# Kernel tuning notes

Hardware: AMD Instinct MI355X
Metric: run time of the kernel (lower is better)

## Reference

```python
import jax, jax.numpy as jnp
import numpy as np

N_NODES = 10000
SEQ_LEN = 50


def setup_inputs() -> dict:
    key = jax.random.key(0)
    ks = jax.random.split(key, 12)
    B, IN, H, E = 2, 128, 64, 160000
    s = 0.05
    return {
        "x": jax.random.normal(ks[0], (B, IN), jnp.float32),
        "src": jax.random.randint(ks[1], (E,), 0, N_NODES, jnp.int32),
        "dst": jax.random.randint(ks[2], (E,), 0, N_NODES, jnp.int32),
        "w_r_w": jax.random.normal(ks[3], (IN, H), jnp.float32) * s,
        "w_r_b": jnp.zeros((H,), jnp.float32),
        "w_z_w": jax.random.normal(ks[4], (IN, H), jnp.float32) * s,
        "w_z_b": jnp.zeros((H,), jnp.float32),
        "w_h_w": jax.random.normal(ks[5], (IN, H), jnp.float32) * s,
        "w_h_b": jnp.zeros((H,), jnp.float32),
        "gcn_w": jax.random.normal(ks[6], (H, H), jnp.float32) * s,
        "gcn_b": jnp.zeros((H,), jnp.float32),
    }


def reference(x, src, dst, w_r_w, w_r_b, w_z_w, w_z_b, w_h_w, w_h_b, gcn_w, gcn_b):
    B = x.shape[0]
    H = gcn_w.shape[0]
    N = N_NODES
    ones = jnp.ones(src.shape, jnp.float32)
    deg_out = jax.ops.segment_sum(ones, src, num_segments=N)
    deg_in = jax.ops.segment_sum(ones, dst, num_segments=N)
    norm_s = jnp.clip(deg_out, 1.0) ** -0.5  # [N]
    norm_d = jnp.clip(deg_in, 1.0) ** -0.5   # [N]

    def gcn(h):  # h: [B, N, H] -> symmetric-normalized GraphConv (DGL norm='both')
        hs = h * norm_s[None, :, None]
        msg = jnp.take(hs, src, axis=1).swapaxes(0, 1)        # [E, B, H]
        agg = jax.ops.segment_sum(msg, dst, num_segments=N)   # [N, B, H]
        agg = (agg * norm_d[:, None, None]).swapaxes(0, 1)    # [B, N, H]
        return agg @ gcn_w + gcn_b

    # time-invariant input projections (x is fixed across timesteps)
    xr = (x @ w_r_w + w_r_b)[:, None, :]  # [B, 1, H]
    xz = (x @ w_z_w + w_z_b)[:, None, :]
    xh = (x @ w_h_w + w_h_b)[:, None, :]

    h0 = jnp.zeros((B, N, H), jnp.float32)

    def step(h, _):
        g = gcn(h)  # identical for all three gate uses
        r = jax.nn.sigmoid(xr + g)
        z = jax.nn.sigmoid(xz + g)
        h_tilde = jnp.tanh(xh + r * g)
        h_new = (1.0 - z) * h + z * h_tilde
        return h_new, h_new

    _, outs = jax.lax.scan(step, h0, None, length=SEQ_LEN)  # [T, B, N, H]
    return outs.transpose(1, 0, 2, 3)                        # [B, T, N, H]
```

## Files before the change

### kernel.cpp

```cpp
#include <hip/hip_runtime.h>
#include <cstdint>
#include <cstddef>

#define NNODES 10000
#define HDIM 64
#define INDIM 128
#define TSTEPS 50

__device__ __forceinline__ float sigmoidf_(float x){ return 1.0f/(1.0f+__expf(-x)); }
__device__ __forceinline__ float tanhf_(float x){ float e=__expf(2.0f*x); return 1.0f-2.0f/(e+1.0f); }

__device__ __forceinline__ uint32_t pack_bf16x2(float a, float b){
  uint32_t ua = __float_as_uint(a), ub = __float_as_uint(b);
  ua = (ua + 0x7fffu + ((ua>>16)&1u)) >> 16;
  ub = (ub + 0x7fffu + ((ub>>16)&1u)) >> 16;
  return ua | (ub<<16);
}

__global__ void hist_kernel(const int* __restrict__ src, const int* __restrict__ dst,
                            int* __restrict__ deg_out, int* __restrict__ deg_in, int E){
  int e = blockIdx.x*blockDim.x + threadIdx.x;
  if (e < E){
    atomicAdd(&deg_out[src[e]], 1);
    atomicAdd(&deg_in[dst[e]], 1);
  }
}

__global__ void scan_kernel(const int* __restrict__ deg_in, const int* __restrict__ deg_out,
                            int* __restrict__ row_off, int* __restrict__ cursor,
                            float* __restrict__ norm_s, float* __restrict__ norm_d){
  __shared__ int part[256];
  int tid = threadIdx.x;
  const int CH = (NNODES + 255)/256;
  int base = tid*CH;
  int local = 0;
  for (int k=0;k<CH;k++){ int n=base+k; if(n<NNODES) local += (deg_in[n]+7)&~7; }
  part[tid]=local;
  __syncthreads();
  if (tid==0){
    int run=0;
    for(int i=0;i<256;i++){ int t=part[i]; part[i]=run; run+=t; }
  }
  __syncthreads();
  int run = part[tid];
  for (int k=0;k<CH;k++){
    int n=base+k;
    if (n<NNODES){
      int di = deg_in[n];
      row_off[n]=run; cursor[n]=run;
      run += (di+7)&~7;
      norm_d[n] = rsqrtf(fmaxf((float)di,1.0f));
      norm_s[n] = rsqrtf(fmaxf((float)deg_out[n],1.0f));
    }
  }
  if (tid==255) row_off[NNODES]=run;
}

__global__ void fill_kernel(const int* __restrict__ src, const int* __restrict__ dst,
                            int* __restrict__ cursor, uint32_t* __restrict__ csrb, int E){
  int e = blockIdx.x*blockDim.x + threadIdx.x;
  if (e<E){
    int pos = atomicAdd(&cursor[dst[e]],1);
    csrb[pos] = (uint32_t)src[e]*256u;
  }
}

__global__ void pad_kernel(const int* __restrict__ row_off, const int* __restrict__ cursor,
                           uint32_t* __restrict__ csrb){
  int n = blockIdx.x*blockDim.x + threadIdx.x;
  if (n < NNODES){
    int q  = cursor[n];
    int qe = row_off[n+1];
    for (; q < qe; ++q) csrb[q] = (uint32_t)NNODES*256u;
  }
}

__global__ void xproj_kernel(const float* __restrict__ x,
                             const float* __restrict__ wr, const float* __restrict__ br,
                             const float* __restrict__ wz, const float* __restrict__ bz,
                             const float* __restrict__ wh, const float* __restrict__ bh,
                             float* __restrict__ xproj){
  int tid = threadIdx.x;
  if (tid >= 384) return;
  int g = tid >> 7; int r = tid & 127; int b = r >> 6; int i = r & 63;
  const float* w  = (g==0)?wr:(g==1)?wz:wh;
  const float* bb = (g==0)?br:(g==1)?bz:bh;
  float s = bb[i];
  for (int k=0;k<INDIM;k++) s = fmaf(x[b*INDIM+k], w[k*HDIM+i], s);
  xproj[g*128 + i*2 + b] = s;
}

__global__ void transpose_w_kernel(const float* __restrict__ gcn_w, float* __restrict__ wT){
  int tid = threadIdx.x;
  for (int k=0;k<16;k++){
    int idx = tid*16 + k;
    int i = idx >> 6, j = idx & 63;
    wT[idx] = gcn_w[j*HDIM + i];
  }
}

#define ACC8(A0,A1,A2,A3,q0,q1,q2,q3,q4,q5,q6,q7) do{ \
  A0.x += __uint_as_float((q0)<<16); A0.y += __uint_as_float((q0)&0xffff0000u); \
  A1.x += __uint_as_float((q1)<<16); A1.y += __uint_as_float((q1)&0xffff0000u); \
  A2.x += __uint_as_float((q2)<<16); A2.y += __uint_as_float((q2)&0xffff0000u); \
  A3.x += __uint_as_float((q3)<<16); A3.y += __uint_as_float((q3)&0xffff0000u); \
  A0.x += __uint_as_float((q4)<<16); A0.y += __uint_as_float((q4)&0xffff0000u); \
  A1.x += __uint_as_float((q5)<<16); A1.y += __uint_as_float((q5)&0xffff0000u); \
  A2.x += __uint_as_float((q6)<<16); A2.y += __uint_as_float((q6)&0xffff0000u); \
  A3.x += __uint_as_float((q7)<<16); A3.y += __uint_as_float((q7)&0xffff0000u); \
}while(0)

#define GATHER8(cp,it,P0,P1,P2,P3,P4,P5,P6,P7) \
  uint4 oa##P0 = (cp)[2*(it)], ob##P0 = (cp)[2*(it)+1]; \
  uint32_t P0 = *(const uint32_t*)(ybb+oa##P0.x); \
  uint32_t P1 = *(const uint32_t*)(ybb+oa##P0.y); \
  uint32_t P2 = *(const uint32_t*)(ybb+oa##P0.z); \
  uint32_t P3 = *(const uint32_t*)(ybb+oa##P0.w); \
  uint32_t P4 = *(const uint32_t*)(ybb+ob##P0.x); \
  uint32_t P5 = *(const uint32_t*)(ybb+ob##P0.y); \
  uint32_t P6 = *(const uint32_t*)(ybb+ob##P0.z); \
  uint32_t P7 = *(const uint32_t*)(ybb+ob##P0.w);

__launch_bounds__(512, 6)
__global__ void step_kernel(const float2* __restrict__ h_in, float2* __restrict__ h_out,
                            const uint32_t* __restrict__ yb_in, uint32_t* __restrict__ yb_out,
                            float* __restrict__ out, int t,
                            const int* __restrict__ row_off, const uint32_t* __restrict__ csrb,
                            const float* __restrict__ norm_d, const float* __restrict__ norm_s,
                            const float* __restrict__ wT, const float* __restrict__ gcn_b,
                            const float2* __restrict__ xproj){
  __shared__ __align__(16) float4 wlds[64][16];
  __shared__ __align__(16) float2 hstage[8][2][64];

  const int tid  = threadIdx.x;
  const int lane = tid & 63;
  const int wv   = tid >> 6;

  {
    const float4* wt4 = (const float4*)wT;
    #pragma unroll
    for (int q=0;q<2;q++){
      int c = tid*2 + q;
      int l = c >> 4, kk = c & 15;
      int swl = (l & 15) ^ (((l>>4)&1) << 2);
      wlds[l][kk ^ swl] = wt4[c];
    }
  }

  const int wid = __builtin_amdgcn_readfirstlane(blockIdx.x*8 + wv);
  const int n0 = wid, n1 = wid + 5000;

  int beg0 = __builtin_amdgcn_readfirstlane(row_off[n0]);
  int end0 = __builtin_amdgcn_readfirstlane(row_off[n0+1]);
  int beg1 = __builtin_amdgcn_readfirstlane(row_off[n1]);
  int end1 = __builtin_amdgcn_readfirstlane(row_off[n1+1]);

  float2 hold0 = h_in[(size_t)n0*HDIM + lane];
  float2 hold1 = h_in[(size_t)n1*HDIM + lane];

  const char* ybb = (const char*)yb_in + (uint32_t)(lane*4);
  const uint4* cp0 = (const uint4*)(csrb + beg0);
  const uint4* cp1 = (const uint4*)(csrb + beg1);
  const int it0 = (end0-beg0)>>3;
  const int it1 = (end1-beg1)>>3;
  const int itc = it0 < it1 ? it0 : it1;

  float2 A0{0.f,0.f},A1{0.f,0.f},A2{0.f,0.f},A3{0.f,0.f};
  float2 B0{0.f,0.f},B1{0.f,0.f},B2{0.f,0.f},B3{0.f,0.f};

  int it = 0;
  #pragma unroll 1
  for (; it<itc; ++it){
    GATHER8(cp0,it,p0,p1,p2,p3,p4,p5,p6,p7);
    GATHER8(cp1,it,q0,q1,q2,q3,q4,q5,q6,q7);
    ACC8(A0,A1,A2,A3,p0,p1,p2,p3,p4,p5,p6,p7);
    ACC8(B0,B1,B2,B3,q0,q1,q2,q3,q4,q5,q6,q7);
  }
  #pragma unroll 1
  for (int ia=it; ia<it0; ++ia){
    GATHER8(cp0,ia,p0,p1,p2,p3,p4,p5,p6,p7);
    ACC8(A0,A1,A2,A3,p0,p1,p2,p3,p4,p5,p6,p7);
  }
  #pragma unroll 1
  for (int ib=it; ib<it1; ++ib){
    GATHER8(cp1,ib,q0,q1,q2,q3,q4,q5,q6,q7);
    ACC8(B0,B1,B2,B3,q0,q1,q2,q3,q4,q5,q6,q7);
  }

  float s00 = (A0.x+A1.x)+(A2.x+A3.x), s01 = (A0.y+A1.y)+(A2.y+A3.y);
  float s10 = (B0.x+B1.x)+(B2.x+B3.x), s11 = (B0.y+B1.y)+(B2.y+B3.y);

  const float  bias = gcn_b[lane];
  const float2 xrv  = xproj[lane];
  const float2 xzv  = xproj[64+lane];
  const float2 xhv  = xproj[128+lane];
  const float  nd0  = norm_d[n0], ns0 = norm_s[n0];
  const float  nd1  = norm_d[n1], ns1 = norm_s[n1];

  float g00 = fmaf(nd0, s00, bias), g01 = fmaf(nd0, s01, bias);
  float g10 = fmaf(nd1, s10, bias), g11 = fmaf(nd1, s11, bias);

  float r00 = sigmoidf_(xrv.x+g00), r01 = sigmoidf_(xrv.y+g01);
  float r10 = sigmoidf_(xrv.x+g10), r11 = sigmoidf_(xrv.y+g11);
  float z00 = sigmoidf_(xzv.x+g00), z01 = sigmoidf_(xzv.y+g01);
  float z10 = sigmoidf_(xzv.x+g10), z11 = sigmoidf_(xzv.y+g11);
  float t00 = tanhf_(xhv.x+r00*g00), t01 = tanhf_(xhv.y+r01*g01);
  float t10 = tanhf_(xhv.x+r10*g10), t11 = tanhf_(xhv.y+r11*g11);
  float h00 = hold0.x + z00*(t00 - hold0.x);
  float h01 = hold0.y + z01*(t01 - hold0.y);
  float h10 = hold1.x + z10*(t10 - hold1.x);
  float h11 = hold1.y + z11*(t11 - hold1.y);

  const size_t NH = (size_t)NNODES*HDIM;
  h_out[(size_t)n0*HDIM + lane] = make_float2(h00,h01);
  h_out[(size_t)n1*HDIM + lane] = make_float2(h10,h11);
  size_t idx0 = (size_t)t*NH + (size_t)n0*HDIM + lane;
  size_t idx1 = (size_t)t*NH + (size_t)n1*HDIM + lane;
  __builtin_nontemporal_store(h00, &out[idx0]);
  __builtin_nontemporal_store(h01, &out[(size_t)TSTEPS*NH + idx0]);
  __builtin_nontemporal_store(h10, &out[idx1]);
  __builtin_nontemporal_store(h11, &out[(size_t)TSTEPS*NH + idx1]);

  hstage[wv][0][lane] = make_float2(h00,h01);
  hstage[wv][1][lane] = make_float2(h10,h11);
  __syncthreads();

  const int sl = (lane & 15) ^ (((lane>>4)&1) << 2);
  const float4* hp0 = (const float4*)hstage[wv][0];
  const float4* hp1 = (const float4*)hstage[wv][1];
  float y00=0.f, y01=0.f, y10=0.f, y11=0.f;
  #pragma unroll
  for (int kk=0;kk<16;kk++){
    float4 w4  = wlds[lane][kk ^ sl];
    float4 ha0 = hp0[2*kk], hb0 = hp0[2*kk+1];
    float4 ha1 = hp1[2*kk], hb1 = hp1[2*kk+1];
    y00 = fmaf(w4.x, ha0.x, y00); y01 = fmaf(w4.x, ha0.y, y01);
    y10 = fmaf(w4.x, ha1.x, y10); y11 = fmaf(w4.x, ha1.y, y11);
    y00 = fmaf(w4.y, ha0.z, y00); y01 = fmaf(w4.y, ha0.w, y01);
    y10 = fmaf(w4.y, ha1.z, y10); y11 = fmaf(w4.y, ha1.w, y11);
    y00 = fmaf(w4.z, hb0.x, y00); y01 = fmaf(w4.z, hb0.y, y01);
    y10 = fmaf(w4.z, hb1.x, y10); y11 = fmaf(w4.z, hb1.y, y11);
    y00 = fmaf(w4.w, hb0.z, y00); y01 = fmaf(w4.w, hb0.w, y01);
    y10 = fmaf(w4.w, hb1.z, y10); y11 = fmaf(w4.w, hb1.w, y11);
  }
  yb_out[(uint32_t)n0*HDIM + lane] = pack_bf16x2(ns0*y00, ns0*y01);
  yb_out[(uint32_t)n1*HDIM + lane] = pack_bf16x2(ns1*y10, ns1*y11);
}

extern "C" void kernel_launch(void* const* d_in, const int* in_sizes, int n_in,
                              void* d_out, int out_size, void* d_ws, size_t ws_size,
                              hipStream_t stream){
  const float* x   = (const float*)d_in[0];
  const int*   src = (const int*)d_in[1];
  const int*   dst = (const int*)d_in[2];
  const float* wr  = (const float*)d_in[3];
  const float* br  = (const float*)d_in[4];
  const float* wz  = (const float*)d_in[5];
  const float* bz  = (const float*)d_in[6];
  const float* wh  = (const float*)d_in[7];
  const float* bh  = (const float*)d_in[8];
  const float* gw  = (const float*)d_in[9];
  const float* gb  = (const float*)d_in[10];
  float* out = (float*)d_out;
  const int E = in_sizes[1];

  char* ws = (char*)d_ws;
  size_t o = 0;
  int*   deg_out = (int*)(ws+o);  o += 10240*4;
  int*   deg_in  = (int*)(ws+o);  o += 10240*4;
  int*   cursor  = (int*)(ws+o);  o += 10240*4;
  int*   row_off = (int*)(ws+o);  o += 10256*4;
  float* norm_s  = (float*)(ws+o); o += 10240*4;
  float* norm_d  = (float*)(ws+o); o += 10240*4;
  const size_t CSRCAP = (size_t)E + 7*NNODES + 16;
  uint32_t* csrb = (uint32_t*)(ws+o);  o += ((CSRCAP*4 + 15) & ~(size_t)15);
  float* xproj   = (float*)(ws+o); o += 512*4;
  float* wT      = (float*)(ws+o); o += 4096*4;
  o = (o + 255) & ~(size_t)255;
  const size_t NHf2 = (size_t)NNODES*HDIM*sizeof(float2);
  const size_t NYB  = (size_t)(NNODES+1)*HDIM*sizeof(uint32_t);
  uint32_t* yb0 = (uint32_t*)(ws+o); o += NYB;
  uint32_t* yb1 = (uint32_t*)(ws+o); o += NYB;
  float2*   h0  = (float2*)(ws+o);   o += NHf2;
  float2*   h1  = (float2*)(ws+o);   o += NHf2;

  hipMemsetAsync(deg_out, 0, 2*10240*4, stream);
  hipMemsetAsync(yb0, 0, 2*NYB + NHf2, stream);

  int eb = (E+255)/256;
  hist_kernel<<<eb,256,0,stream>>>(src,dst,deg_out,deg_in,E);
  scan_kernel<<<1,256,0,stream>>>(deg_in,deg_out,row_off,cursor,norm_s,norm_d);
  fill_kernel<<<eb,256,0,stream>>>(src,dst,cursor,csrb,E);
  pad_kernel<<<(NNODES+255)/256,256,0,stream>>>(row_off,cursor,csrb);
  xproj_kernel<<<1,384,0,stream>>>(x,wr,br,wz,bz,wh,bh,xproj);
  transpose_w_kernel<<<1,256,0,stream>>>(gw,wT);

  float2* hin = h0;  float2* hout = h1;
  uint32_t* ybin = yb0; uint32_t* ybout = yb1;
  for (int t=0;t<TSTEPS;t++){
    step_kernel<<<625,512,0,stream>>>(hin,hout,ybin,ybout,out,t,row_off,csrb,
                                      norm_d,norm_s,wT,gb,(const float2*)xproj);
    float2* tf = hin; hin = hout; hout = tf;
    uint32_t* tb = ybin; ybin = ybout; ybout = tb;
  }
}
```

Measured before the change: 989.5 us.

## Use fixed-width 32-slot dense neighbor table with overflow, one node per wave

```diff
diff --git a/kernel.cpp b/kernel.cpp
--- a/kernel.cpp
+++ b/kernel.cpp
@@ -6,6 +6,7 @@
 #define HDIM 64
 #define INDIM 128
 #define TSTEPS 50
+#define SENTOFF ((uint32_t)NNODES*256u)
 
 __device__ __forceinline__ float sigmoidf_(float x){ return 1.0f/(1.0f+__expf(-x)); }
 __device__ __forceinline__ float tanhf_(float x){ float e=__expf(2.0f*x); return 1.0f-2.0f/(e+1.0f); }
@@ -71,8 +72,19 @@
   if (n < NNODES){
     int q  = cursor[n];
     int qe = row_off[n+1];
-    for (; q < qe; ++q) csrb[q] = (uint32_t)NNODES*256u;
-  }
+    for (; q < qe; ++q) csrb[q] = SENTOFF;
+  }
+}
+
+__global__ void dense_kernel(const int* __restrict__ row_off, const uint32_t* __restrict__ csrb,
+                             uint32_t* __restrict__ csrd, uint32_t* __restrict__ ovc){
+  int idx = blockIdx.x*blockDim.x + threadIdx.x;
+  if (idx >= NNODES*32) return;
+  int n = idx >> 5, j = idx & 31;
+  int beg = row_off[n], end = row_off[n+1];
+  int pd = end - beg;
+  csrd[idx] = (j < pd) ? csrb[beg+j] : SENTOFF;
+  if (j==0) ovc[n] = (pd > 32) ? (uint32_t)((pd-32)>>3) : 0u;
 }
 
 __global__ void xproj_kernel(const float* __restrict__ x,
@@ -125,12 +137,13 @@
 __global__ void step_kernel(const float2* __restrict__ h_in, float2* __restrict__ h_out,
                             const uint32_t* __restrict__ yb_in, uint32_t* __restrict__ yb_out,
                             float* __restrict__ out, int t,
+                            const uint32_t* __restrict__ csrd, const uint32_t* __restrict__ ovc,
                             const int* __restrict__ row_off, const uint32_t* __restrict__ csrb,
                             const float* __restrict__ norm_d, const float* __restrict__ norm_s,
                             const float* __restrict__ wT, const float* __restrict__ gcn_b,
                             const float2* __restrict__ xproj){
   __shared__ __align__(16) float4 wlds[64][16];
-  __shared__ __align__(16) float2 hstage[8][2][64];
+  __shared__ __align__(16) float2 hstage[8][64];
 
   const int tid  = threadIdx.x;
   const int lane = tid & 63;
@@ -147,104 +160,106 @@
     }
   }
 
-  const int wid = __builtin_amdgcn_readfirstlane(blockIdx.x*8 + wv);
-  const int n0 = wid, n1 = wid + 5000;
-
-  int beg0 = __builtin_amdgcn_readfirstlane(row_off[n0]);
-  int end0 = __builtin_amdgcn_readfirstlane(row_off[n0+1]);
-  int beg1 = __builtin_amdgcn_readfirstlane(row_off[n1]);
-  int end1 = __builtin_amdgcn_readfirstlane(row_off[n1+1]);
-
-  float2 hold0 = h_in[(size_t)n0*HDIM + lane];
-  float2 hold1 = h_in[(size_t)n1*HDIM + lane];
+  const int n = __builtin_amdgcn_readfirstlane(blockIdx.x*8 + wv);
 
   const char* ybb = (const char*)yb_in + (uint32_t)(lane*4);
-  const uint4* cp0 = (const uint4*)(csrb + beg0);
-  const uint4* cp1 = (const uint4*)(csrb + beg1);
-  const int it0 = (end0-beg0)>>3;
-  const int it1 = (end1-beg1)>>3;
-  const int itc = it0 < it1 ? it0 : it1;
+  const uint4* op = (const uint4*)(csrd + (uint32_t)n*32u);
+  uint4 o0=op[0], o1=op[1], o2=op[2], o3=op[3];
+  uint4 o4=op[4], o5=op[5], o6=op[6], o7=op[7];
+
+  float2 hold = h_in[(size_t)n*HDIM + lane];
+
+  uint32_t g0  = *(const uint32_t*)(ybb+o0.x);
+  uint32_t g1  = *(const uint32_t*)(ybb+o0.y);
+  uint32_t g2  = *(const uint32_t*)(ybb+o0.z);
+  uint32_t g3  = *(const uint32_t*)(ybb+o0.w);
+  uint32_t g4  = *(const uint32_t*)(ybb+o1.x);
+  uint32_t g5  = *(const uint32_t*)(ybb+o1.y);
+  uint32_t g6  = *(const uint32_t*)(ybb+o1.z);
+  uint32_t g7  = *(const uint32_t*)(ybb+o1.w);
+  uint32_t g8  = *(const uint32_t*)(ybb+o2.x);
+  uint32_t g9  = *(const uint32_t*)(ybb+o2.y);
+  uint32_t g10 = *(const uint32_t*)(ybb+o2.z);
+  uint32_t g11 = *(const uint32_t*)(ybb+o2.w);
+  uint32_t g12 = *(const uint32_t*)(ybb+o3.x);
+  uint32_t g13 = *(const uint32_t*)(ybb+o3.y);
+  uint32_t g14 = *(const uint32_t*)(ybb+o3.z);
+  uint32_t g15 = *(const uint32_t*)(ybb+o3.w);
+  uint32_t g16 = *(const uint32_t*)(ybb+o4.x);
+  uint32_t g17 = *(const uint32_t*)(ybb+o4.y);
+  uint32_t g18 = *(const uint32_t*)(ybb+o4.z);
+  uint32_t g19 = *(const uint32_t*)(ybb+o4.w);
+  uint32_t g20 = *(const uint32_t*)(ybb+o5.x);
+  uint32_t g21 = *(const uint32_t*)(ybb+o5.y);
+  uint32_t g22 = *(const uint32_t*)(ybb+o5.z);
+  uint32_t g23 = *(const uint32_t*)(ybb+o5.w);
+  uint32_t g24 = *(const uint32_t*)(ybb+o6.x);
+  uint32_t g25 = *(const uint32_t*)(ybb+o6.y);
+  uint32_t g26 = *(const uint32_t*)(ybb+o6.z);
+  uint32_t g27 = *(const uint32_t*)(ybb+o6.w);
+  uint32_t g28 = *(const uint32_t*)(ybb+o7.x);
+  uint32_t g29 = *(const uint32_t*)(ybb+o7.y);
+  uint32_t g30 = *(const uint32_t*)(ybb+o7.z);
+  uint32_t g31 = *(const uint32_t*)(ybb+o7.w);
 
   float2 A0{0.f,0.f},A1{0.f,0.f},A2{0.f,0.f},A3{0.f,0.f};
-  float2 B0{0.f,0.f},B1{0.f,0.f},B2{0.f,0.f},B3{0.f,0.f};
-
-  int it = 0;
-  #pragma unroll 1
-  for (; it<itc; ++it){
-    GATHER8(cp0,it,p0,p1,p2,p3,p4,p5,p6,p7);
-    GATHER8(cp1,it,q0,q1,q2,q3,q4,q5,q6,q7);
-    ACC8(A0,A1,A2,A3,p0,p1,p2,p3,p4,p5,p6,p7);
-    ACC8(B0,B1,B2,B3,q0,q1,q2,q3,q4,q5,q6,q7);
-  }
-  #pragma unroll 1
-  for (int ia=it; ia<it0; ++ia){
-    GATHER8(cp0,ia,p0,p1,p2,p3,p4,p5,p6,p7);
-    ACC8(A0,A1,A2,A3,p0,p1,p2,p3,p4,p5,p6,p7);
-  }
-  #pragma unroll 1
-  for (int ib=it; ib<it1; ++ib){
-    GATHER8(cp1,ib,q0,q1,q2,q3,q4,q5,q6,q7);
-    ACC8(B0,B1,B2,B3,q0,q1,q2,q3,q4,q5,q6,q7);
-  }
-
-  float s00 = (A0.x+A1.x)+(A2.x+A3.x), s01 = (A0.y+A1.y)+(A2.y+A3.y);
-  float s10 = (B0.x+B1.x)+(B2.x+B3.x), s11 = (B0.y+B1.y)+(B2.y+B3.y);
+  ACC8(A0,A1,A2,A3,g0,g1,g2,g3,g4,g5,g6,g7);
+  ACC8(A0,A1,A2,A3,g8,g9,g10,g11,g12,g13,g14,g15);
+  ACC8(A0,A1,A2,A3,g16,g17,g18,g19,g20,g21,g22,g23);
+  ACC8(A0,A1,A2,A3,g24,g25,g26,g27,g28,g29,g30,g31);
+
+  uint32_t ov = __builtin_amdgcn_readfirstlane(ovc[n]);
+  if (ov){
+    int beg = __builtin_amdgcn_readfirstlane(row_off[n]);
+    const uint4* cp = (const uint4*)(csrb + beg + 32);
+    #pragma unroll 1
+    for (uint32_t r=0;r<ov;r++){
+      GATHER8(cp,r,p0,p1,p2,p3,p4,p5,p6,p7);
+      ACC8(A0,A1,A2,A3,p0,p1,p2,p3,p4,p5,p6,p7);
+    }
+  }
+
+  float s0 = (A0.x+A1.x)+(A2.x+A3.x);
+  float s1 = (A0.y+A1.y)+(A2.y+A3.y);
 
   const float  bias = gcn_b[lane];
   const float2 xrv  = xproj[lane];
   const float2 xzv  = xproj[64+lane];
   const float2 xhv  = xproj[128+lane];
-  const float  nd0  = norm_d[n0], ns0 = norm_s[n0];
-  const float  nd1  = norm_d[n1], ns1 = norm_s[n1];
-
-  float g00 = fmaf(nd0, s00, bias), g01 = fmaf(nd0, s01, bias);
-  float g10 = fmaf(nd1, s10, bias), g11 = fmaf(nd1, s11, bias);
-
-  float r00 = sigmoidf_(xrv.x+g00), r01 = sigmoidf_(xrv.y+g01);
-  float r10 = sigmoidf_(xrv.x+g10), r11 = sigmoidf_(xrv.y+g11);
-  float z00 = sigmoidf_(xzv.x+g00), z01 = sigmoidf_(xzv.y+g01);
-  float z10 = sigmoidf_(xzv.x+g10), z11 = sigmoidf_(xzv.y+g11);
-  float t00 = tanhf_(xhv.x+r00*g00), t01 = tanhf_(xhv.y+r01*g01);
-  float t10 = tanhf_(xhv.x+r10*g10), t11 = tanhf_(xhv.y+r11*g11);
-  float h00 = hold0.x + z00*(t00 - hold0.x);
-  float h01 = hold0.y + z01*(t01 - hold0.y);
-  float h10 = hold1.x + z10*(t10 - hold1.x);
-  float h11 = hold1.y + z11*(t11 - hold1.y);
+  const float  nd   = norm_d[n], ns = norm_s[n];
+
+  float g0f = fmaf(nd, s0, bias);
+  float g1f = fmaf(nd, s1, bias);
+
+  float r0 = sigmoidf_(xrv.x+g0f), r1 = sigmoidf_(xrv.y+g1f);
+  float z0 = sigmoidf_(xzv.x+g0f), z1 = sigmoidf_(xzv.y+g1f);
+  float t0 = tanhf_(xhv.x+r0*g0f), t1 = tanhf_(xhv.y+r1*g1f);
+  float hn0 = hold.x + z0*(t0 - hold.x);
+  float hn1 = hold.y + z1*(t1 - hold.y);
 
   const size_t NH = (size_t)NNODES*HDIM;
-  h_out[(size_t)n0*HDIM + lane] = make_float2(h00,h01);
-  h_out[(size_t)n1*HDIM + lane] = make_float2(h10,h11);
-  size_t idx0 = (size_t)t*NH + (size_t)n0*HDIM + lane;
-  size_t idx1 = (size_t)t*NH + (size_t)n1*HDIM + lane;
-  __builtin_nontemporal_store(h00, &out[idx0]);
-  __builtin_nontemporal_store(h01, &out[(size_t)TSTEPS*NH + idx0]);
-  __builtin_nontemporal_store(h10, &out[idx1]);
-  __builtin_nontemporal_store(h11, &out[(size_t)TSTEPS*NH + idx1]);
-
-  hstage[wv][0][lane] = make_float2(h00,h01);
-  hstage[wv][1][lane] = make_float2(h10,h11);
+  h_out[(size_t)n*HDIM + lane] = make_float2(hn0,hn1);
+  size_t idx = (size_t)t*NH + (size_t)n*HDIM + lane;
+  __builtin_nontemporal_store(hn0, &out[idx]);
+  __builtin_nontemporal_store(hn1, &out[(size_t)TSTEPS*NH + idx]);
+
+  hstage[wv][lane] = make_float2(hn0,hn1);
   __syncthreads();
 
   const int sl = (lane & 15) ^ (((lane>>4)&1) << 2);
-  const float4* hp0 = (const float4*)hstage[wv][0];
-  const float4* hp1 = (const float4*)hstage[wv][1];
-  float y00=0.f, y01=0.f, y10=0.f, y11=0.f;
+  const float4* hp = (const float4*)hstage[wv];
+  float y0 = 0.f, y1 = 0.f;
   #pragma unroll
   for (int kk=0;kk<16;kk++){
-    float4 w4  = wlds[lane][kk ^ sl];
-    float4 ha0 = hp0[2*kk], hb0 = hp0[2*kk+1];
-    float4 ha1 = hp1[2*kk], hb1 = hp1[2*kk+1];
-    y00 = fmaf(w4.x, ha0.x, y00); y01 = fmaf(w4.x, ha0.y, y01);
-    y10 = fmaf(w4.x, ha1.x, y10); y11 = fmaf(w4.x, ha1.y, y11);
-    y00 = fmaf(w4.y, ha0.z, y00); y01 = fmaf(w4.y, ha0.w, y01);
-    y10 = fmaf(w4.y, ha1.z, y10); y11 = fmaf(w4.y, ha1.w, y11);
-    y00 = fmaf(w4.z, hb0.x, y00); y01 = fmaf(w4.z, hb0.y, y01);
-    y10 = fmaf(w4.z, hb1.x, y10); y11 = fmaf(w4.z, hb1.y, y11);
-    y00 = fmaf(w4.w, hb0.z, y00); y01 = fmaf(w4.w, hb0.w, y01);
-    y10 = fmaf(w4.w, hb1.z, y10); y11 = fmaf(w4.w, hb1.w, y11);
-  }
-  yb_out[(uint32_t)n0*HDIM + lane] = pack_bf16x2(ns0*y00, ns0*y01);
-  yb_out[(uint32_t)n1*HDIM + lane] = pack_bf16x2(ns1*y10, ns1*y11);
+    float4 w4 = wlds[lane][kk ^ sl];
+    float4 ha = hp[2*kk];
+    float4 hb = hp[2*kk+1];
+    y0 = fmaf(w4.x, ha.x, y0); y1 = fmaf(w4.x, ha.y, y1);
+    y0 = fmaf(w4.y, ha.z, y0); y1 = fmaf(w4.y, ha.w, y1);
+    y0 = fmaf(w4.z, hb.x, y0); y1 = fmaf(w4.z, hb.y, y1);
+    y0 = fmaf(w4.w, hb.z, y0); y1 = fmaf(w4.w, hb.w, y1);
+  }
+  yb_out[(uint32_t)n*HDIM + lane] = pack_bf16x2(ns*y0, ns*y1);
 }
 
 extern "C" void kernel_launch(void* const* d_in, const int* in_sizes, int n_in,
@@ -274,6 +289,8 @@
   float* norm_d  = (float*)(ws+o); o += 10240*4;
   const size_t CSRCAP = (size_t)E + 7*NNODES + 16;
   uint32_t* csrb = (uint32_t*)(ws+o);  o += ((CSRCAP*4 + 15) & ~(size_t)15);
+  uint32_t* csrd = (uint32_t*)(ws+o);  o += (size_t)NNODES*32*4;
+  uint32_t* ovc  = (uint32_t*)(ws+o);  o += (size_t)NNODES*4;
   float* xproj   = (float*)(ws+o); o += 512*4;
   float* wT      = (float*)(ws+o); o += 4096*4;
   o = (o + 255) & ~(size_t)255;
@@ -292,14 +309,16 @@
   scan_kernel<<<1,256,0,stream>>>(deg_in,deg_out,row_off,cursor,norm_s,norm_d);
   fill_kernel<<<eb,256,0,stream>>>(src,dst,cursor,csrb,E);
   pad_kernel<<<(NNODES+255)/256,256,0,stream>>>(row_off,cursor,csrb);
+  dense_kernel<<<(NNODES*32+255)/256,256,0,stream>>>(row_off,csrb,csrd,ovc);
   xproj_kernel<<<1,384,0,stream>>>(x,wr,br,wz,bz,wh,bh,xproj);
   transpose_w_kernel<<<1,256,0,stream>>>(gw,wT);
 
   float2* hin = h0;  float2* hout = h1;
   uint32_t* ybin = yb0; uint32_t* ybout = yb1;
   for (int t=0;t<TSTEPS;t++){
-    step_kernel<<<625,512,0,stream>>>(hin,hout,ybin,ybout,out,t,row_off,csrb,
-                                      norm_d,norm_s,wT,gb,(const float2*)xproj);
+    step_kernel<<<1250,512,0,stream>>>(hin,hout,ybin,ybout,out,t,csrd,ovc,
+                                       row_off,csrb,norm_d,norm_s,wT,gb,
+                                       (const float2*)xproj);
     float2* tf = hin; hin = hout; hout = tf;
     uint32_t* tb = ybin; ybin = ybout; ybout = tb;
   }
```

Result: faster. 968.8 us (-2.1%).
